# Optimization experiments

Measured on AMD Instinct MI355X. Metric: run time of the kernel, lower is better.

Reference implementation:

```python
import jax, jax.numpy as jnp
import numpy as np

K = 20
LN_EPS = 1e-5
NEG_SLOPE = 0.2


def _knn(x, k):
    # x: (B, C, N) -> idx (B, N, k) of k nearest neighbors (incl. self)
    xx = jnp.sum(x * x, axis=1)                      # (B, N)
    inner = jnp.einsum('bcn,bcm->bnm', x, x)         # (B, N, N)
    pd = -xx[:, :, None] + 2.0 * inner - xx[:, None, :]  # -||xi-xj||^2
    return jax.lax.top_k(pd, k)[1]


def _layernorm(h, g, b):
    m = jnp.mean(h, axis=-1, keepdims=True)
    v = jnp.var(h, axis=-1, keepdims=True)
    return (h - m) * jax.lax.rsqrt(v + LN_EPS) * g + b


def _edge_conv(x, k, W, g, b):
    # x: (B, C, N); W: (Cout, 2C) 1x1 conv; returns (B, Cout, N)
    idx = _knn(x, k)                                 # (B, N, k)
    xt = jnp.transpose(x, (0, 2, 1))                 # (B, N, C)
    nbr = jax.vmap(lambda f, i: f[i])(xt, idx)       # (B, N, k, C)
    ctr = xt[:, :, None, :]                          # (B, N, 1, C)
    comb = jnp.concatenate([nbr - ctr, jnp.broadcast_to(ctr, nbr.shape)], axis=-1)
    h = jnp.einsum('oc,bnkc->bnko', W, comb)         # (B, N, k, Cout)
    h = _layernorm(h, g, b)
    h = jnp.where(h >= 0, h, NEG_SLOPE * h)          # LeakyReLU(0.2)
    return jnp.transpose(jnp.max(h, axis=2), (0, 2, 1))


def _normalize(x):
    # x: (B, 3, N) -> center and scale to unit max radius
    c = jnp.mean(x, axis=2, keepdims=True)
    xc = x - c
    md = jnp.max(jnp.sqrt(jnp.sum(xc * xc, axis=1)), axis=1)[:, None, None]
    return xc / (md + 1e-8)


def setup_inputs() -> dict:
    key = jax.random.key(0)
    ks = jax.random.split(key, 13)
    f32 = jnp.float32
    x = jax.random.normal(ks[0], (4, 3, 4096), dtype=f32)
    def conv_w(k_, cout, cin):
        return jax.random.normal(k_, (cout, cin), dtype=f32) * (1.0 / np.sqrt(cin))
    return {
        'x': x,
        'W1': conv_w(ks[1], 16, 6),  'g1': jnp.ones((16,), f32), 'b1': jnp.zeros((16,), f32),
        'W2': conv_w(ks[2], 16, 32), 'g2': jnp.ones((16,), f32), 'b2': jnp.zeros((16,), f32),
        'W3': conv_w(ks[3], 32, 32), 'g3': jnp.ones((32,), f32), 'b3': jnp.zeros((32,), f32),
        'W4': conv_w(ks[4], 64, 64), 'g4': jnp.ones((64,), f32), 'b4': jnp.zeros((64,), f32),
    }


def reference(x, W1, g1, b1, W2, g2, b2, W3, g3, b3, W4, g4, b4):
    xn = _normalize(x)
    x1 = _edge_conv(xn, K, W1, g1, b1)   # (B, 16, N)
    x2 = _edge_conv(x1, K, W2, g2, b2)   # (B, 16, N)
    x3 = _edge_conv(x2, K, W3, g3, b3)   # (B, 32, N)
    x4 = _edge_conv(x3, K, W4, g4, b4)   # (B, 64, N)
    x_cat = jnp.concatenate([x1, x2, x3, x4], axis=1)  # (B, 128, N)
    return jnp.max(x_cat, axis=-1)                     # (B, 128)
```

## Files before the change

kernel.cpp:

```cpp
#include <hip/hip_runtime.h>

#define K_NN 20
#define LN_EPS 1e-5f
#define NEG_SLOPE 0.2f
#define BUFSZ 15
#define ARRSZ 32

__device__ __forceinline__ unsigned ordf(float f){
  unsigned u = __float_as_uint(f);
  return u ^ (((unsigned)((int)u >> 31)) | 0x80000000u);
}
__device__ __forceinline__ float unordf(unsigned u){
  unsigned m = ((int)u < 0) ? 0x80000000u : 0xFFFFFFFFu;
  return __uint_as_float(u ^ m);
}

__device__ __forceinline__ void ce_desc(unsigned long long &a, unsigned long long &b){
  unsigned long long mx = a>b ? a : b;
  unsigned long long mn = a>b ? b : a;
  a = mx; b = mn;
}

__device__ __forceinline__ void sort16_desc(unsigned long long (&v)[16]){
  #pragma unroll
  for (int k=2;k<=16;k<<=1){
    #pragma unroll
    for (int j=k>>1;j>0;j>>=1){
      #pragma unroll
      for (int i=0;i<16;++i){
        int l = i ^ j;
        if (l > i){
          if ((i & k) == 0) ce_desc(v[i], v[l]);
          else              ce_desc(v[l], v[i]);
        }
      }
    }
  }
}

__device__ __forceinline__ void bmerge32_desc(unsigned long long (&v)[32]){
  #pragma unroll
  for (int d=16; d>0; d>>=1){
    #pragma unroll
    for (int i=0;i<32;++i){
      if ((i & d) == 0) ce_desc(v[i], v[i|d]);
    }
  }
}

__global__ __launch_bounds__(1024) void normalize_kernel(const float* __restrict__ x,
                                                         float* __restrict__ xn, int N){
  __shared__ float red[1024];
  __shared__ float ms[4];
  const int b = blockIdx.x;
  const int t = threadIdx.x;
  const float* xb = x + (size_t)b*3*N;
  float s0=0.f,s1=0.f,s2=0.f;
  for (int n=t;n<N;n+=1024){ s0+=xb[n]; s1+=xb[N+n]; s2+=xb[2*N+n]; }
  red[t]=s0; __syncthreads();
  for(int o=512;o>0;o>>=1){ if(t<o) red[t]+=red[t+o]; __syncthreads(); }
  if(!t) ms[0]=red[0]/(float)N; __syncthreads();
  red[t]=s1; __syncthreads();
  for(int o=512;o>0;o>>=1){ if(t<o) red[t]+=red[t+o]; __syncthreads(); }
  if(!t) ms[1]=red[0]/(float)N; __syncthreads();
  red[t]=s2; __syncthreads();
  for(int o=512;o>0;o>>=1){ if(t<o) red[t]+=red[t+o]; __syncthreads(); }
  if(!t) ms[2]=red[0]/(float)N; __syncthreads();
  const float m0=ms[0], m1=ms[1], m2=ms[2];
  float mx=0.f;
  for (int n=t;n<N;n+=1024){
    float a=xb[n]-m0, c1=xb[N+n]-m1, c2=xb[2*N+n]-m2;
    mx = fmaxf(mx, a*a+c1*c1+c2*c2);
  }
  red[t]=mx; __syncthreads();
  for(int o=512;o>0;o>>=1){ if(t<o) red[t]=fmaxf(red[t],red[t+o]); __syncthreads(); }
  if(!t) ms[3]=sqrtf(red[0])+1e-8f; __syncthreads();
  const float md=ms[3];
  for (int n=t;n<N;n+=1024){
    float a=xb[n]-m0, c1=xb[N+n]-m1, c2=xb[2*N+n]-m2;
    float4 v; v.x=a/md; v.y=c1/md; v.z=c2/md; v.w=0.f;
    reinterpret_cast<float4*>(xn)[(size_t)b*N+n]=v;
  }
}

template<int CP4>
__global__ __launch_bounds__(256) void xx_kernel(const float* __restrict__ feat,
                                                 float* __restrict__ xx, int total){
  int i = blockIdx.x*256 + threadIdx.x;
  if (i>=total) return;
  const float4* p = reinterpret_cast<const float4*>(feat) + (size_t)i*CP4;
  float s=0.f;
  #pragma unroll
  for (int j=0;j<CP4;++j){
    float4 v=p[j];
    s=fmaf(v.x,v.x,s); s=fmaf(v.y,v.y,s); s=fmaf(v.z,v.z,s); s=fmaf(v.w,v.w,s);
  }
  xx[i]=s;
}

template<int CP4>
__global__ __launch_bounds__(512,4) void knn_kernel(const float* __restrict__ feat,
                                                    const float* __restrict__ xx,
                                                    unsigned* __restrict__ pd32,
                                                    unsigned short* __restrict__ pi16,
                                                    int N){
  __shared__ unsigned long long sbuf[BUFSZ*512];
  const int ng = N>>6;
  const int s  = blockIdx.x & 1;
  const int gi = blockIdx.x >> 1;
  const int b  = gi / ng;
  const int n0 = (gi % ng) << 6;
  const int tid = threadIdx.x;
  const int lane = tid & 63;
  const int w = __builtin_amdgcn_readfirstlane(tid >> 6);
  const int bN = b*N;
  const int n = n0 + lane;
  const float4* fb = reinterpret_cast<const float4*>(feat);
  float4 own[CP4];
  #pragma unroll
  for (int i=0;i<CP4;++i) own[i] = fb[(size_t)(bN+n)*CP4 + i];
  const float xxn = xx[bN+n];

  unsigned long long arr[ARRSZ];
  #pragma unroll
  for (int i=0;i<ARRSZ;++i) arr[i] = (unsigned long long)(ARRSZ-1-i);
  unsigned long long rmin = 0ull;
  int cnt = 0;

  auto do_flush = [&](){
    unsigned long long bv[16];
    #pragma unroll
    for (int q=0;q<BUFSZ;++q){
      unsigned long long v = sbuf[q*512 + tid];
      bv[q] = (q < cnt) ? v : 0ull;
    }
    bv[15] = 0ull;
    sort16_desc(bv);
    #pragma unroll
    for (int i=16;i<32;++i){
      unsigned long long t2 = bv[31-i];
      arr[i] = arr[i] > t2 ? arr[i] : t2;
    }
    bmerge32_desc(arr);
    rmin = arr[K_NN-1];
    cnt = 0;
  };

  const int m0 = s*(N>>1) + w*(N>>4);
  const int pairs = N>>5;
  for (int tt=0; tt<pairs; ++tt){
    const int mA = m0 + 2*tt;
    const int mB = mA + 1;
    const float4* cpA = fb + (size_t)(bN+mA)*CP4;
    const float4* cpB = fb + (size_t)(bN+mB)*CP4;
    float a0=0.f, a1=0.f, b0=0.f, b1=0.f;
    #pragma unroll
    for (int i=0;i<CP4;++i){
      float4 ca = cpA[i];
      float4 cb = cpB[i];
      a0 = fmaf(own[i].x,ca.x,a0); b0 = fmaf(own[i].x,cb.x,b0);
      a1 = fmaf(own[i].y,ca.y,a1); b1 = fmaf(own[i].y,cb.y,b1);
      a0 = fmaf(own[i].z,ca.z,a0); b0 = fmaf(own[i].z,cb.z,b0);
      a1 = fmaf(own[i].w,ca.w,a1); b1 = fmaf(own[i].w,cb.w,b1);
    }
    const float pdA = fmaf(2.f, a0+a1, -xxn) - xx[bN+mA];
    const float pdB = fmaf(2.f, b0+b1, -xxn) - xx[bN+mB];
    const unsigned long long keyA = ((unsigned long long)ordf(pdA)<<32) | (unsigned)(mA ^ 0xFFFF);
    const unsigned long long keyB = ((unsigned long long)ordf(pdB)<<32) | (unsigned)(mB ^ 0xFFFF);
    if (keyA > rmin){ sbuf[cnt*512 + tid] = keyA; ++cnt; }
    if (keyB > rmin){ sbuf[cnt*512 + tid] = keyB; ++cnt; }
    if (__ballot(cnt >= BUFSZ-1)) do_flush();
  }
  if (__ballot(cnt > 0)) do_flush();

  __syncthreads();
  unsigned* lkh = (unsigned*)sbuf;
  unsigned short* lki = (unsigned short*)(((char*)sbuf)+40960);
  #pragma unroll
  for (int i=0;i<K_NN;++i){
    lkh[((w*K_NN+i)<<6)+lane] = (unsigned)(arr[i]>>32);
    lki[((w*K_NN+i)<<6)+lane] = (unsigned short)(arr[i]&0xFFFFu);
  }
  __syncthreads();
  if (tid < 64){
    const int l = tid;
    unsigned long long heads[8];
    #pragma unroll
    for (int j=0;j<8;++j){
      int q0=((j*K_NN)<<6)+l;
      heads[j]=((unsigned long long)lkh[q0]<<16)|(unsigned long long)lki[q0];
    }
    unsigned long long pk=0ull;
    const size_t pbase = ((size_t)(bN+n0+l)*2 + s)*K_NN;
    for (int kk=0;kk<K_NN;++kk){
      unsigned long long best=heads[0]; int bj=0;
      #pragma unroll
      for (int j=1;j<8;++j){ bool gg=heads[j]>best; best=gg?heads[j]:best; bj=gg?j:bj; }
      pd32[pbase+kk] = (unsigned)(best>>16);
      pi16[pbase+kk] = (unsigned short)(best & 0xFFFFu);
      unsigned pos = (unsigned)((pk>>(bj*5))&0x1Ful)+1u;
      pk += (1ull<<(bj*5));
      unsigned long long nv = 0ull;
      if (pos<K_NN){
        int q1=((bj*K_NN+(int)pos)<<6)+l;
        nv=((unsigned long long)lkh[q1]<<16)|(unsigned long long)lki[q1];
      }
      #pragma unroll
      for (int j=0;j<8;++j) heads[j]=(j==bj)?nv:heads[j];
    }
  }
}

__global__ __launch_bounds__(256) void knn_merge_kernel(const unsigned* __restrict__ pd32,
                                                        const unsigned short* __restrict__ pi16,
                                                        int* __restrict__ idx_out, int total){
  int i = blockIdx.x*256 + threadIdx.x;
  if (i>=total) return;
  const unsigned* d0 = pd32 + (size_t)i*2*K_NN;
  const unsigned short* i0 = pi16 + (size_t)i*2*K_NN;
  const unsigned* d1 = d0 + K_NN;
  const unsigned short* i1 = i0 + K_NN;
  int a=0, c=0;
  int* op = idx_out + (size_t)i*K_NN;
  #pragma unroll 4
  for (int k=0;k<K_NN;++k){
    unsigned long long k0 = ((unsigned long long)d0[a]<<16) | i0[a];
    unsigned long long k1 = ((unsigned long long)d1[c]<<16) | i1[c];
    bool t = k0 > k1;
    unsigned long long best = t ? k0 : k1;
    op[k] = (int)(((unsigned)best & 0xFFFFu) ^ 0xFFFFu);
    a += t; c += !t;
  }
}

template<int CIN,int CP4,int O>
__global__ __launch_bounds__(256) void ctr_half_kernel(const float* __restrict__ feat,
                                                       const float* __restrict__ W,
                                                       float* __restrict__ h0, int total){
  int i = blockIdx.x*256+threadIdx.x;
  if (i>=total) return;
  const float4* p = reinterpret_cast<const float4*>(feat)+(size_t)i*CP4;
  float c[CP4*4];
  #pragma unroll
  for (int j=0;j<CP4;++j){
    float4 v=p[j];
    c[4*j+0]=v.x; c[4*j+1]=v.y; c[4*j+2]=v.z; c[4*j+3]=v.w;
  }
  float* hp = h0 + (size_t)i*O;
  #pragma unroll
  for (int o=0;o<O;++o){
    const float* wr = W + o*(2*CIN) + CIN;
    float a=0.f;
    #pragma unroll
    for (int cc=0;cc<CIN;++cc) a=fmaf(wr[cc],c[cc],a);
    hp[o]=a;
  }
}

template<int CIN,int CP4,int O>
__global__ __launch_bounds__(320) void edge_kernel(const float* __restrict__ feat,
      const int* __restrict__ knn_idx, const float* __restrict__ h0,
      const float* __restrict__ W, const float* __restrict__ g, const float* __restrict__ bb,
      float* __restrict__ outf, int N){
  __shared__ unsigned ob[16*O];
  const int t = threadIdx.x;
  const int p = t/K_NN, k = t - p*K_NN;
  const int b = blockIdx.y;
  const int n = blockIdx.x*16 + p;
  const int bN = b*N;
  for (int v=t; v<16*O; v+=320) ob[v]=0u;
  __syncthreads();
  const int m = knn_idx[(size_t)(bN+n)*K_NN + k];
  const float4* fb = reinterpret_cast<const float4*>(feat);
  float d[CP4*4];
  #pragma unroll
  for (int j=0;j<CP4;++j){
    float4 a = fb[(size_t)(bN+m)*CP4+j];
    float4 c = fb[(size_t)(bN+n)*CP4+j];
    d[4*j+0]=a.x-c.x; d[4*j+1]=a.y-c.y; d[4*j+2]=a.z-c.z; d[4*j+3]=a.w-c.w;
  }
  float h[O];
  const float4* hp = reinterpret_cast<const float4*>(h0 + (size_t)(bN+n)*O);
  #pragma unroll
  for (int j=0;j<O/4;++j){ float4 v=hp[j]; h[4*j]=v.x; h[4*j+1]=v.y; h[4*j+2]=v.z; h[4*j+3]=v.w; }
  #pragma unroll
  for (int o=0;o<O;++o){
    const float* wr = W + o*(2*CIN);
    float a=h[o];
    #pragma unroll
    for (int cc=0;cc<CIN;++cc) a=fmaf(wr[cc],d[cc],a);
    h[o]=a;
  }
  float mean=0.f;
  #pragma unroll
  for (int o=0;o<O;++o) mean+=h[o];
  mean *= (1.f/(float)O);
  float var=0.f;
  #pragma unroll
  for (int o=0;o<O;++o){ float dd=h[o]-mean; var=fmaf(dd,dd,var); }
  var *= (1.f/(float)O);
  const float r = rsqrtf(var+LN_EPS);
  #pragma unroll
  for (int o=0;o<O;++o){
    float hv = (h[o]-mean)*r*g[o]+bb[o];
    hv = (hv>=0.f)? hv : NEG_SLOPE*hv;
    atomicMax(&ob[p*O+o], ordf(hv));
  }
  __syncthreads();
  for (int v=t; v<16*O; v+=320){
    int pp=v/O, oo=v-pp*O;
    outf[(size_t)(bN+blockIdx.x*16+pp)*O+oo]=unordf(ob[v]);
  }
}

__global__ __launch_bounds__(256) void final_max_kernel(const float* __restrict__ x1,
    const float* __restrict__ x2, const float* __restrict__ x3, const float* __restrict__ x4,
    float* __restrict__ out, int N){
  __shared__ float red[256];
  const int L=blockIdx.x, b=blockIdx.y;
  const float* f; int O, off;
  if (L==0){f=x1;O=16;off=0;}
  else if (L==1){f=x2;O=16;off=16;}
  else if (L==2){f=x3;O=32;off=32;}
  else {f=x4;O=64;off=64;}
  const int t=threadIdx.x;
  const int c=t%O, s=t/O, S=256/O;
  float acc=-3.402823466e38f;
  for (int n=s;n<N;n+=S) acc=fmaxf(acc, f[(size_t)(b*N+n)*O+c]);
  red[t]=acc; __syncthreads();
  if (t<O){
    float a=red[t];
    for (int ss=1;ss<S;++ss) a=fmaxf(a,red[ss*O+t]);
    out[b*128+off+t]=a;
  }
}

extern "C" void kernel_launch(void* const* d_in, const int* in_sizes, int n_in,
                              void* d_out, int out_size, void* d_ws, size_t ws_size,
                              hipStream_t stream){
  const float* x  = (const float*)d_in[0];
  const float* W1 = (const float*)d_in[1];  const float* g1=(const float*)d_in[2];  const float* b1=(const float*)d_in[3];
  const float* W2 = (const float*)d_in[4];  const float* g2=(const float*)d_in[5];  const float* b2=(const float*)d_in[6];
  const float* W3 = (const float*)d_in[7];  const float* g3=(const float*)d_in[8];  const float* b3=(const float*)d_in[9];
  const float* W4 = (const float*)d_in[10]; const float* g4=(const float*)d_in[11]; const float* b4=(const float*)d_in[12];
  float* out=(float*)d_out;
  const int B=4;
  const int N=in_sizes[0]/(3*B);
  const int BN=B*N;

  char* ws=(char*)d_ws;
  size_t off=0;
  auto alloc=[&](size_t bytes)->void*{ void* p=ws+off; off=(off+bytes+255)&~(size_t)255; return p; };
  float* xn =(float*)alloc((size_t)BN*4*4);
  float* x1 =(float*)alloc((size_t)BN*16*4);
  float* x2 =(float*)alloc((size_t)BN*16*4);
  float* x3 =(float*)alloc((size_t)BN*32*4);
  float* x4 =(float*)alloc((size_t)BN*64*4);
  float* xxb=(float*)alloc((size_t)BN*4);
  int*   knn=(int*)  alloc((size_t)BN*K_NN*4);
  float* h0 =(float*)alloc((size_t)BN*64*4);

  unsigned* pd32 = (unsigned*)h0;
  unsigned short* pi16 = (unsigned short*)((char*)h0 + (size_t)BN*2*K_NN*4);

  dim3 pb((BN+255)/256), tb(256);
  dim3 kb(B*(N/64)*2), kt(512);
  dim3 eb(N/16,B), et(320);

  normalize_kernel<<<dim3(B),dim3(1024),0,stream>>>(x,xn,N);

  xx_kernel<1><<<pb,tb,0,stream>>>(xn,xxb,BN);
  knn_kernel<1><<<kb,kt,0,stream>>>(xn,xxb,pd32,pi16,N);
  knn_merge_kernel<<<pb,tb,0,stream>>>(pd32,pi16,knn,BN);
  ctr_half_kernel<3,1,16><<<pb,tb,0,stream>>>(xn,W1,h0,BN);
  edge_kernel<3,1,16><<<eb,et,0,stream>>>(xn,knn,h0,W1,g1,b1,x1,N);

  xx_kernel<4><<<pb,tb,0,stream>>>(x1,xxb,BN);
  knn_kernel<4><<<kb,kt,0,stream>>>(x1,xxb,pd32,pi16,N);
  knn_merge_kernel<<<pb,tb,0,stream>>>(pd32,pi16,knn,BN);
  ctr_half_kernel<16,4,16><<<pb,tb,0,stream>>>(x1,W2,h0,BN);
  edge_kernel<16,4,16><<<eb,et,0,stream>>>(x1,knn,h0,W2,g2,b2,x2,N);

  xx_kernel<4><<<pb,tb,0,stream>>>(x2,xxb,BN);
  knn_kernel<4><<<kb,kt,0,stream>>>(x2,xxb,pd32,pi16,N);
  knn_merge_kernel<<<pb,tb,0,stream>>>(pd32,pi16,knn,BN);
  ctr_half_kernel<16,4,32><<<pb,tb,0,stream>>>(x2,W3,h0,BN);
  edge_kernel<16,4,32><<<eb,et,0,stream>>>(x2,knn,h0,W3,g3,b3,x3,N);

  xx_kernel<8><<<pb,tb,0,stream>>>(x3,xxb,BN);
  knn_kernel<8><<<kb,kt,0,stream>>>(x3,xxb,pd32,pi16,N);
  knn_merge_kernel<<<pb,tb,0,stream>>>(pd32,pi16,knn,BN);
  ctr_half_kernel<32,8,64><<<pb,tb,0,stream>>>(x3,W4,h0,BN);
  edge_kernel<32,8,64><<<eb,et,0,stream>>>(x3,knn,h0,W4,g4,b4,x4,N);

  final_max_kernel<<<dim3(4,B),dim3(256),0,stream>>>(x1,x2,x3,x4,out,N);
}
```

Before: 1.042 ms.

## Split KNN candidate scan four ways and merge via in-block and 4-way merge

The KNN kernel now splits the candidate range into four slices per query group instead of two, doubling the grid. The per-thread staging buffer shrinks and launch bounds are raised so more blocks can be resident. Per-wave partial top-k lists are merged in shared memory in two phases, because of the smaller buffer. The separate merge kernel now does a 4-way merge of larger partial lists. The aim is more parallelism and occupancy in the dominant KNN stage, at the cost of more partial-result traffic, more merge work and possible register spills.

Result: slower. 1.271 ms (+22.0%).

```diff
diff --git a/kernel.cpp b/kernel.cpp
--- a/kernel.cpp
+++ b/kernel.cpp
@@ -3,7 +3,7 @@
 #define K_NN 20
 #define LN_EPS 1e-5f
 #define NEG_SLOPE 0.2f
-#define BUFSZ 15
+#define BUFSZ 13
 #define ARRSZ 32
 
 __device__ __forceinline__ unsigned ordf(float f){
@@ -99,15 +99,15 @@
 }
 
 template<int CP4>
-__global__ __launch_bounds__(512,4) void knn_kernel(const float* __restrict__ feat,
+__global__ __launch_bounds__(512,8) void knn_kernel(const float* __restrict__ feat,
                                                     const float* __restrict__ xx,
                                                     unsigned* __restrict__ pd32,
                                                     unsigned short* __restrict__ pi16,
                                                     int N){
   __shared__ unsigned long long sbuf[BUFSZ*512];
   const int ng = N>>6;
-  const int s  = blockIdx.x & 1;
-  const int gi = blockIdx.x >> 1;
+  const int s  = blockIdx.x & 3;
+  const int gi = blockIdx.x >> 2;
   const int b  = gi / ng;
   const int n0 = (gi % ng) << 6;
   const int tid = threadIdx.x;
@@ -130,11 +130,10 @@
   auto do_flush = [&](){
     unsigned long long bv[16];
     #pragma unroll
-    for (int q=0;q<BUFSZ;++q){
-      unsigned long long v = sbuf[q*512 + tid];
+    for (int q=0;q<16;++q){
+      unsigned long long v = (q<BUFSZ) ? sbuf[q*512 + tid] : 0ull;
       bv[q] = (q < cnt) ? v : 0ull;
     }
-    bv[15] = 0ull;
     sort16_desc(bv);
     #pragma unroll
     for (int i=16;i<32;++i){
@@ -146,8 +145,8 @@
     cnt = 0;
   };
 
-  const int m0 = s*(N>>1) + w*(N>>4);
-  const int pairs = N>>5;
+  const int m0 = s*(N>>2) + w*(N>>5);
+  const int pairs = N>>6;
   for (int tt=0; tt<pairs; ++tt){
     const int mA = m0 + 2*tt;
     const int mB = mA + 1;
@@ -173,40 +172,91 @@
   }
   if (__ballot(cnt > 0)) do_flush();
 
-  __syncthreads();
-  unsigned* lkh = (unsigned*)sbuf;
-  unsigned short* lki = (unsigned short*)(((char*)sbuf)+40960);
-  #pragma unroll
-  for (int i=0;i<K_NN;++i){
-    lkh[((w*K_NN+i)<<6)+lane] = (unsigned)(arr[i]>>32);
-    lki[((w*K_NN+i)<<6)+lane] = (unsigned short)(arr[i]&0xFFFFu);
+  unsigned*       h4 = (unsigned*)sbuf;
+  unsigned short* i4 = (unsigned short*)(((char*)sbuf)+20480);
+  unsigned*       h1 = (unsigned*)(((char*)sbuf)+30720);
+  unsigned short* i1 = (unsigned short*)(((char*)sbuf)+35840);
+
+  __syncthreads();
+  if (w < 4){
+    #pragma unroll
+    for (int i=0;i<K_NN;++i){
+      h4[((w*K_NN+i)<<6)+lane] = (unsigned)(arr[i]>>32);
+      i4[((w*K_NN+i)<<6)+lane] = (unsigned short)(arr[i]&0xFFFFu);
+    }
   }
   __syncthreads();
   if (tid < 64){
     const int l = tid;
-    unsigned long long heads[8];
-    #pragma unroll
-    for (int j=0;j<8;++j){
+    unsigned long long heads[4];
+    #pragma unroll
+    for (int j=0;j<4;++j){
       int q0=((j*K_NN)<<6)+l;
-      heads[j]=((unsigned long long)lkh[q0]<<16)|(unsigned long long)lki[q0];
-    }
-    unsigned long long pk=0ull;
-    const size_t pbase = ((size_t)(bN+n0+l)*2 + s)*K_NN;
+      heads[j]=((unsigned long long)h4[q0]<<16)|(unsigned long long)i4[q0];
+    }
+    unsigned pk=0;
     for (int kk=0;kk<K_NN;++kk){
       unsigned long long best=heads[0]; int bj=0;
       #pragma unroll
-      for (int j=1;j<8;++j){ bool gg=heads[j]>best; best=gg?heads[j]:best; bj=gg?j:bj; }
-      pd32[pbase+kk] = (unsigned)(best>>16);
-      pi16[pbase+kk] = (unsigned short)(best & 0xFFFFu);
-      unsigned pos = (unsigned)((pk>>(bj*5))&0x1Ful)+1u;
-      pk += (1ull<<(bj*5));
+      for (int j=1;j<4;++j){ bool gg=heads[j]>best; best=gg?heads[j]:best; bj=gg?j:bj; }
+      h1[(kk<<6)+l] = (unsigned)(best>>16);
+      i1[(kk<<6)+l] = (unsigned short)(best&0xFFFFu);
+      unsigned pos = ((pk>>(bj*8))&0xFFu)+1u;
+      pk += (1u<<(bj*8));
       unsigned long long nv = 0ull;
       if (pos<K_NN){
         int q1=((bj*K_NN+(int)pos)<<6)+l;
-        nv=((unsigned long long)lkh[q1]<<16)|(unsigned long long)lki[q1];
+        nv=((unsigned long long)h4[q1]<<16)|(unsigned long long)i4[q1];
       }
       #pragma unroll
-      for (int j=0;j<8;++j) heads[j]=(j==bj)?nv:heads[j];
+      for (int j=0;j<4;++j) heads[j]=(j==bj)?nv:heads[j];
+    }
+  }
+  __syncthreads();
+  if (w >= 4){
+    const int ws = w-4;
+    #pragma unroll
+    for (int i=0;i<K_NN;++i){
+      h4[((ws*K_NN+i)<<6)+lane] = (unsigned)(arr[i]>>32);
+      i4[((ws*K_NN+i)<<6)+lane] = (unsigned short)(arr[i]&0xFFFFu);
+    }
+  }
+  __syncthreads();
+  if (tid < 64){
+    const int l = tid;
+    unsigned long long heads[4];
+    #pragma unroll
+    for (int j=0;j<4;++j){
+      int q0=((j*K_NN)<<6)+l;
+      heads[j]=((unsigned long long)h4[q0]<<16)|(unsigned long long)i4[q0];
+    }
+    unsigned long long hC = ((unsigned long long)h1[l]<<16)|(unsigned long long)i1[l];
+    unsigned pk=0;
+    int posC = 0;
+    const size_t pbase = ((size_t)(bN+n0+l)*4 + s)*K_NN;
+    for (int kk=0;kk<K_NN;++kk){
+      unsigned long long best=heads[0]; int bj=0;
+      #pragma unroll
+      for (int j=1;j<4;++j){ bool gg=heads[j]>best; best=gg?heads[j]:best; bj=gg?j:bj; }
+      { bool gg=hC>best; best=gg?hC:best; bj=gg?4:bj; }
+      pd32[pbase+kk] = (unsigned)(best>>16);
+      pi16[pbase+kk] = (unsigned short)(best&0xFFFFu);
+      if (bj < 4){
+        unsigned pos = ((pk>>(bj*8))&0xFFu)+1u;
+        pk += (1u<<(bj*8));
+        unsigned long long nv = 0ull;
+        if (pos<K_NN){
+          int q1=((bj*K_NN+(int)pos)<<6)+l;
+          nv=((unsigned long long)h4[q1]<<16)|(unsigned long long)i4[q1];
+        }
+        #pragma unroll
+        for (int j=0;j<4;++j) heads[j]=(j==bj)?nv:heads[j];
+      } else {
+        ++posC;
+        hC = 0ull;
+        if (posC<K_NN)
+          hC = ((unsigned long long)h1[(posC<<6)+l]<<16)|(unsigned long long)i1[(posC<<6)+l];
+      }
     }
   }
 }
@@ -216,20 +266,25 @@
                                                         int* __restrict__ idx_out, int total){
   int i = blockIdx.x*256 + threadIdx.x;
   if (i>=total) return;
-  const unsigned* d0 = pd32 + (size_t)i*2*K_NN;
-  const unsigned short* i0 = pi16 + (size_t)i*2*K_NN;
-  const unsigned* d1 = d0 + K_NN;
-  const unsigned short* i1 = i0 + K_NN;
-  int a=0, c=0;
+  unsigned long long h[4];
+  #pragma unroll
+  for (int j=0;j<4;++j)
+    h[j] = ((unsigned long long)pd32[((size_t)i*4+j)*K_NN]<<16) | pi16[((size_t)i*4+j)*K_NN];
+  unsigned pk=0;
   int* op = idx_out + (size_t)i*K_NN;
-  #pragma unroll 4
   for (int k=0;k<K_NN;++k){
-    unsigned long long k0 = ((unsigned long long)d0[a]<<16) | i0[a];
-    unsigned long long k1 = ((unsigned long long)d1[c]<<16) | i1[c];
-    bool t = k0 > k1;
-    unsigned long long best = t ? k0 : k1;
+    unsigned long long best=h[0]; int bj=0;
+    #pragma unroll
+    for (int j=1;j<4;++j){ bool gg=h[j]>best; best=gg?h[j]:best; bj=gg?j:bj; }
     op[k] = (int)(((unsigned)best & 0xFFFFu) ^ 0xFFFFu);
-    a += t; c += !t;
+    unsigned pos = ((pk>>(bj*8))&0xFFu)+1u;
+    pk += (1u<<(bj*8));
+    unsigned long long nv = 0ull;
+    if (pos<K_NN)
+      nv = ((unsigned long long)pd32[((size_t)i*4+bj)*K_NN+pos]<<16)
+         | pi16[((size_t)i*4+bj)*K_NN+pos];
+    #pragma unroll
+    for (int j=0;j<4;++j) h[j]=(j==bj)?nv:h[j];
   }
 }
 
@@ -359,12 +414,11 @@
   float* xxb=(float*)alloc((size_t)BN*4);
   int*   knn=(int*)  alloc((size_t)BN*K_NN*4);
   float* h0 =(float*)alloc((size_t)BN*64*4);
-
-  unsigned* pd32 = (unsigned*)h0;
-  unsigned short* pi16 = (unsigned short*)((char*)h0 + (size_t)BN*2*K_NN*4);
+  unsigned* pd32 = (unsigned*)alloc((size_t)BN*4*K_NN*4);
+  unsigned short* pi16 = (unsigned short*)h0;
 
   dim3 pb((BN+255)/256), tb(256);
-  dim3 kb(B*(N/64)*2), kt(512);
+  dim3 kb(B*(N/64)*4), kt(512);
   dim3 eb(N/16,B), et(320);
 
   normalize_kernel<<<dim3(B),dim3(1024),0,stream>>>(x,xn,N);
```
